# Kernel tuning notes

Hardware: AMD Instinct MI355X
Metric: run time of the kernel (lower is better)

Reference implementation:

```python
import jax, jax.numpy as jnp
import numpy as np

_NF4_LUT = jnp.array([-1.0, -0.6961928, -0.525073, -0.39491748, -0.28444138,
                      -0.18477343, -0.09105602, 0.0, 0.07958029, 0.1609302,
                      0.2461123, 0.33791524, 0.44070983, 0.56261897,
                      0.72295684, 1.0], dtype=jnp.float32)

IN_FEATURES = 4096


def dequantize_nf4(weight_q, scale, in_dim):
    # weight_q: (out, in_dim//2) bytes (stored as int32, values 0..255)
    high = (weight_q >> 4) & 15
    low = weight_q & 15
    n_out = weight_q.shape[0]
    # interleave: [h0, l0, h1, l1, ...] matching torch's 0::2 / 1::2 assignment
    idx = jnp.stack([high, low], axis=-1).reshape(n_out, -1)[:, :in_dim]
    return _NF4_LUT[idx] * scale[:, None]  # (out, in) float32


def setup_inputs() -> dict:
    key = jax.random.key(0)
    k1, k2, k3, k4 = jax.random.split(key, 4)
    x = jax.random.normal(k1, (2, 2048, 4096), dtype=jnp.float32)
    weight_q = jax.random.randint(k2, (11008, 2048), 0, 256, dtype=jnp.int32)
    scale = jax.random.uniform(k3, (11008,), dtype=jnp.float32)
    bias = jax.random.normal(k4, (11008,), dtype=jnp.float32)
    return {"x": x, "weight_q": weight_q, "scale": scale, "bias": bias}


def reference(x, weight_q, scale, bias):
    w = dequantize_nf4(weight_q, scale, IN_FEATURES)  # (out, in)
    # F.linear: x @ w.T + bias
    return jnp.einsum('bsi,oi->bso', x, w.astype(x.dtype)) + bias
```

## Files before the change

### kernel.cpp

```cpp
#include <hip/hip_runtime.h>
#include <stdint.h>

#define M_DIM 4096
#define K_DIM 4096
#define N_DIM 11008
#define KW_DIM 2048

typedef __bf16 bf16x8 __attribute__((ext_vector_type(8)));
typedef float  f32x4  __attribute__((ext_vector_type(4)));

typedef __attribute__((address_space(1))) const void gv_t;
typedef __attribute__((address_space(3))) void lv_t;

__device__ inline unsigned int bf16_rne_bits(float f) {
    unsigned int u = __float_as_uint(f);
    return (u + 0x7FFFu + ((u >> 16) & 1u)) >> 16;
}
__device__ inline unsigned int pack_bf16_pair(float lo, float hi) {
    return bf16_rne_bits(lo) | (bf16_rne_bits(hi) << 16);
}

#define NF4_INIT  {-1.0f, -0.6961928f, -0.525073f, -0.39491748f, \
                   -0.28444138f, -0.18477343f, -0.09105602f, 0.0f, \
                   0.07958029f, 0.1609302f, 0.2461123f, 0.33791524f, \
                   0.44070983f, 0.56261897f, 0.72295684f, 1.0f}

__global__ __launch_bounds__(256)
void dequant_w(const int4* __restrict__ Wq4, uint4* __restrict__ Wb4)
{
    __shared__ unsigned int lutr[256 * 32];
    const int t = threadIdx.x;
    {
        const float LUT[16] = NF4_INIT;
        const int c0 = t & 31;
        #pragma unroll
        for (int j = 0; j < 32; ++j) {
            const int e = (t >> 5) * 32 + j;
            lutr[e * 32 + c0] = pack_bf16_pair(LUT[(e >> 4) & 15], LUT[e & 15]);
        }
    }
    __syncthreads();
    const int c = t & 31;
    size_t gid = (size_t)blockIdx.x * 256 + t;
    const size_t stride = 2752u * 256u;
    #pragma unroll
    for (int it = 0; it < 8; ++it) {
        int4 w = Wq4[gid];
        uint4 o;
        o.x = lutr[(w.x & 255) * 32 + c];
        o.y = lutr[(w.y & 255) * 32 + c];
        o.z = lutr[(w.z & 255) * 32 + c];
        o.w = lutr[(w.w & 255) * 32 + c];
        Wb4[gid] = o;
        gid += stride;
    }
}

__global__ __launch_bounds__(256)
void convert_x(const float4* __restrict__ X4, uint4* __restrict__ Xb4)
{
    size_t gid = (size_t)blockIdx.x * 256 + threadIdx.x;
    float4 a = X4[gid * 2];
    float4 b = X4[gid * 2 + 1];
    uint4 o;
    o.x = pack_bf16_pair(a.x, a.y);
    o.y = pack_bf16_pair(a.z, a.w);
    o.z = pack_bf16_pair(b.x, b.y);
    o.w = pack_bf16_pair(b.z, b.w);
    Xb4[gid] = o;
}

constexpr int GBM = 256, GBN = 256, GBK = 32;
constexpr int NKT = K_DIM / GBK;
constexpr int NT2 = N_DIM / GBN;
constexpr int GRID2 = (M_DIM / GBM) * NT2;

__global__ __launch_bounds__(512, 2)
void gemm_8ph(const unsigned short* __restrict__ Xb, const unsigned short* __restrict__ Wb,
              const float* __restrict__ scale, const float* __restrict__ bias,
              float* __restrict__ Out)
{
    __shared__ __align__(16) char lds[131072];
    char* const ldsA = lds;
    char* const ldsB = lds + 65536;

    const int t = threadIdx.x;
    const int lane = t & 63;
    const int wv = t >> 6;
    const int wr = wv >> 2;
    const int wc = wv & 3;
    const int l16 = lane & 15, quad = lane >> 4;

    const int bid = blockIdx.x;
    const int wg = (bid & 7) * (GRID2 / 8) + (bid >> 3);
    const int m0 = (wg / NT2) * GBM;
    const int n0 = (wg % NT2) * GBN;

    const int sw  = ((quad ^ ((l16 >> 1) & 3)) << 4);
    const int a_rd = (wr * 128 + l16) * 64 + sw;
    const int b_rd = (wc * 64  + l16) * 64 + sw;

    const int srow  = t >> 2;
    const int sslot = (t & 3) ^ ((t >> 3) & 3);
    const unsigned short* sA = Xb + (size_t)(m0 + srow) * K_DIM + sslot * 8;
    const unsigned short* sB = Wb + (size_t)(n0 + srow) * K_DIM + sslot * 8;
    const int sdst = t * 16;

    f32x4 acc[8][4];
    #pragma unroll
    for (int i = 0; i < 8; ++i)
        #pragma unroll
        for (int j = 0; j < 4; ++j)
            acc[i][j] = f32x4{0.f, 0.f, 0.f, 0.f};

    #pragma unroll
    for (int k0 = 0; k0 < 3; ++k0) {
        char* Ad = ldsA + k0 * 16384;
        char* Bd = ldsB + k0 * 16384;
        __builtin_amdgcn_global_load_lds((gv_t*)(sA + k0 * 32),
                                         (lv_t*)(Ad + sdst), 16, 0, 0);
        __builtin_amdgcn_global_load_lds((gv_t*)(sA + k0 * 32 + (size_t)128 * K_DIM),
                                         (lv_t*)(Ad + 8192 + sdst), 16, 0, 0);
        __builtin_amdgcn_global_load_lds((gv_t*)(sB + k0 * 32),
                                         (lv_t*)(Bd + sdst), 16, 0, 0);
        __builtin_amdgcn_global_load_lds((gv_t*)(sB + k0 * 32 + (size_t)128 * K_DIM),
                                         (lv_t*)(Bd + 8192 + sdst), 16, 0, 0);
    }
    asm volatile("s_waitcnt vmcnt(8)" ::: "memory");
    __builtin_amdgcn_s_barrier();

    #pragma unroll 4
    for (int kt = 0; kt < NKT; ++kt) {
        const char* Ab = ldsA + (kt & 3) * 16384;
        const char* Bb = ldsB + (kt & 3) * 16384;
        const int ktS = (kt + 3 < NKT) ? (kt + 3) : (NKT - 1);
        char* AdS = ldsA + ((kt + 3) & 3) * 16384;
        char* BdS = ldsB + ((kt + 3) & 3) * 16384;

        bf16x8 af[4], bfr[4];

        #pragma unroll
        for (int i = 0; i < 4; ++i)
            af[i] = *reinterpret_cast<const bf16x8*>(Ab + a_rd + i * 1024);
        #pragma unroll
        for (int j = 0; j < 4; ++j)
            bfr[j] = *reinterpret_cast<const bf16x8*>(Bb + b_rd + j * 1024);
        __builtin_amdgcn_global_load_lds((gv_t*)(sA + ktS * 32),
                                         (lv_t*)(AdS + sdst), 16, 0, 0);
        __builtin_amdgcn_global_load_lds((gv_t*)(sA + ktS * 32 + (size_t)128 * K_DIM),
                                         (lv_t*)(AdS + 8192 + sdst), 16, 0, 0);
        __builtin_amdgcn_s_barrier();
        asm volatile("s_waitcnt lgkmcnt(0)" ::: "memory");
        __builtin_amdgcn_s_setprio(1);
        #pragma unroll
        for (int i = 0; i < 4; ++i)
            #pragma unroll
            for (int j = 0; j < 4; ++j)
                acc[i][j] = __builtin_amdgcn_mfma_f32_16x16x32_bf16(af[i], bfr[j], acc[i][j], 0, 0, 0);
        __builtin_amdgcn_s_setprio(0);
        __builtin_amdgcn_s_barrier();

        #pragma unroll
        for (int i = 0; i < 4; ++i)
            af[i] = *reinterpret_cast<const bf16x8*>(Ab + a_rd + 4096 + i * 1024);
        __builtin_amdgcn_global_load_lds((gv_t*)(sB + ktS * 32),
                                         (lv_t*)(BdS + sdst), 16, 0, 0);
        __builtin_amdgcn_global_load_lds((gv_t*)(sB + ktS * 32 + (size_t)128 * K_DIM),
                                         (lv_t*)(BdS + 8192 + sdst), 16, 0, 0);
        __builtin_amdgcn_s_barrier();
        asm volatile("s_waitcnt lgkmcnt(0)" ::: "memory");
        __builtin_amdgcn_s_setprio(1);
        #pragma unroll
        for (int i = 0; i < 4; ++i)
            #pragma unroll
            for (int j = 0; j < 4; ++j)
                acc[4 + i][j] = __builtin_amdgcn_mfma_f32_16x16x32_bf16(af[i], bfr[j], acc[4 + i][j], 0, 0, 0);
        __builtin_amdgcn_s_setprio(0);
        asm volatile("s_waitcnt vmcnt(8)" ::: "memory");
        __builtin_amdgcn_s_barrier();
    }

    asm volatile("s_waitcnt vmcnt(0)" ::: "memory");

    #pragma unroll
    for (int j = 0; j < 4; ++j) {
        const int n = n0 + wc * 64 + j * 16 + l16;
        const float s  = scale[n];
        const float bz = bias[n];
        #pragma unroll
        for (int ii = 0; ii < 8; ++ii) {
            const int m = m0 + wr * 128 + ii * 16 + quad * 4;
            float* op = Out + (size_t)m * N_DIM + n;
            #pragma unroll
            for (int r = 0; r < 4; ++r)
                op[(size_t)r * N_DIM] = acc[ii][j][r] * s + bz;
        }
    }
}

constexpr int BM = 128, BN = 128, BK = 64;
constexpr int F_LDK = BK + 8;
__global__ __launch_bounds__(256, 2)
void nf4_gemm_fused(const float* __restrict__ X, const int* __restrict__ Wq,
                    const float* __restrict__ scale, const float* __restrict__ bias,
                    float* __restrict__ Out)
{
    __shared__ __align__(16) unsigned short As[BM * F_LDK];
    __shared__ __align__(16) unsigned short Bs[BN * F_LDK];
    __shared__ unsigned int lut2[256];

    const int t = threadIdx.x;
    const int ntiles = N_DIM / BN;
    const int mtile = blockIdx.x / ntiles;
    const int ntile = blockIdx.x % ntiles;
    const int m0 = mtile * BM, n0 = ntile * BN;

    {
        const float LUT[16] = NF4_INIT;
        lut2[t] = pack_bf16_pair(LUT[(t >> 4) & 15], LUT[t & 15]);
    }

    const int lane = t & 63;
    const int wv = t >> 6;
    const int wr = wv >> 1, wc = wv & 1;
    const int l16 = lane & 15, quad = lane >> 4;

    const int a_r = t >> 4, a_c = (t & 15) * 4;
    const int b_r = t >> 3, b_c = (t & 7) * 4;

    const float* aptr = X + (m0 + a_r) * K_DIM + a_c;
    const int*   bptr = Wq + (n0 + b_r) * KW_DIM + b_c;

    f32x4 acc[4][4];
    #pragma unroll
    for (int i = 0; i < 4; ++i)
        #pragma unroll
        for (int j = 0; j < 4; ++j)
            acc[i][j] = f32x4{0.f, 0.f, 0.f, 0.f};

    for (int kt = 0; kt < K_DIM / BK; ++kt) {
        float4 av[8];
        int4   bv[4];
        #pragma unroll
        for (int i = 0; i < 8; ++i)
            av[i] = *reinterpret_cast<const float4*>(aptr + i * 16 * K_DIM);
        #pragma unroll
        for (int i = 0; i < 4; ++i)
            bv[i] = *reinterpret_cast<const int4*>(bptr + i * 32 * KW_DIM);
        aptr += BK;
        bptr += BK / 2;

        __syncthreads();

        #pragma unroll
        for (int i = 0; i < 8; ++i) {
            uint2 p;
            p.x = pack_bf16_pair(av[i].x, av[i].y);
            p.y = pack_bf16_pair(av[i].z, av[i].w);
            *reinterpret_cast<uint2*>(&As[(a_r + i * 16) * F_LDK + a_c]) = p;
        }
        #pragma unroll
        for (int i = 0; i < 4; ++i) {
            uint4 q;
            q.x = lut2[bv[i].x & 255];
            q.y = lut2[bv[i].y & 255];
            q.z = lut2[bv[i].z & 255];
            q.w = lut2[bv[i].w & 255];
            *reinterpret_cast<uint4*>(&Bs[(b_r + i * 32) * F_LDK + b_c * 2]) = q;
        }
        __syncthreads();

        #pragma unroll
        for (int ks = 0; ks < 2; ++ks) {
            bf16x8 af[4], bfr[4];
            const int kb = ks * 32 + quad * 8;
            #pragma unroll
            for (int i = 0; i < 4; ++i)
                af[i] = *reinterpret_cast<const bf16x8*>(&As[(wr * 64 + i * 16 + l16) * F_LDK + kb]);
            #pragma unroll
            for (int j = 0; j < 4; ++j)
                bfr[j] = *reinterpret_cast<const bf16x8*>(&Bs[(wc * 64 + j * 16 + l16) * F_LDK + kb]);
            #pragma unroll
            for (int i = 0; i < 4; ++i)
                #pragma unroll
                for (int j = 0; j < 4; ++j)
                    acc[i][j] = __builtin_amdgcn_mfma_f32_16x16x32_bf16(af[i], bfr[j], acc[i][j], 0, 0, 0);
        }
    }

    #pragma unroll
    for (int j = 0; j < 4; ++j) {
        const int n = n0 + wc * 64 + j * 16 + l16;
        const float s  = scale[n];
        const float bz = bias[n];
        #pragma unroll
        for (int i = 0; i < 4; ++i) {
            const int m = m0 + wr * 64 + i * 16 + quad * 4;
            float* op = Out + (size_t)m * N_DIM + n;
            #pragma unroll
            for (int r = 0; r < 4; ++r)
                op[(size_t)r * N_DIM] = acc[i][j][r] * s + bz;
        }
    }
}

extern "C" void kernel_launch(void* const* d_in, const int* in_sizes, int n_in,
                              void* d_out, int out_size, void* d_ws, size_t ws_size,
                              hipStream_t stream) {
    const float* X     = (const float*)d_in[0];
    const int*   Wq    = (const int*)d_in[1];
    const float* scale = (const float*)d_in[2];
    const float* bias  = (const float*)d_in[3];
    float* Out = (float*)d_out;

    const size_t WB_BYTES = (size_t)N_DIM * K_DIM * 2;
    const size_t XB_BYTES = (size_t)M_DIM * K_DIM * 2;

    if (ws_size >= WB_BYTES + XB_BYTES) {
        unsigned short* Wb = (unsigned short*)d_ws;
        unsigned short* Xb = (unsigned short*)((char*)d_ws + WB_BYTES);
        dequant_w<<<2752, 256, 0, stream>>>((const int4*)Wq, (uint4*)Wb);
        convert_x<<<8192, 256, 0, stream>>>((const float4*)X, (uint4*)Xb);
        gemm_8ph<<<GRID2, 512, 0, stream>>>(Xb, Wb, scale, bias, Out);
    } else {
        nf4_gemm_fused<<<(M_DIM / BM) * (N_DIM / BN), 256, 0, stream>>>(X, Wq, scale, bias, Out);
    }
}
```

Before: 611.1 us.

## Switch GEMM to BK=64 double-buffered LDS pipeline with 8-slot XOR swizzle

Replaces the 4-stage BK=32 LDS ring, which had split phases and several barriers per k-step, with a 2-stage BK=64 double buffer. Each k-step prefetches the next 64-wide tile of A and B into the other buffer, then runs two K-halves of MFMAs with a single barrier at the end. The LDS swizzle changes to an 8-slot XOR pattern to suit 128-byte rows. This halves the loop trip count and cuts barrier and waitcnt overhead, at the cost of shallower prefetch and less latency hiding.

```diff
diff --git a/kernel.cpp b/kernel.cpp
--- a/kernel.cpp
+++ b/kernel.cpp
@@ -70,15 +70,15 @@
     Xb4[gid] = o;
 }
 
-constexpr int GBM = 256, GBN = 256, GBK = 32;
+constexpr int GBM = 256, GBN = 256, GBK = 64;
 constexpr int NKT = K_DIM / GBK;
 constexpr int NT2 = N_DIM / GBN;
 constexpr int GRID2 = (M_DIM / GBM) * NT2;
 
 __global__ __launch_bounds__(512, 2)
-void gemm_8ph(const unsigned short* __restrict__ Xb, const unsigned short* __restrict__ Wb,
-              const float* __restrict__ scale, const float* __restrict__ bias,
-              float* __restrict__ Out)
+void gemm_bk64(const unsigned short* __restrict__ Xb, const unsigned short* __restrict__ Wb,
+               const float* __restrict__ scale, const float* __restrict__ bias,
+               float* __restrict__ Out)
 {
     __shared__ __align__(16) char lds[131072];
     char* const ldsA = lds;
@@ -96,12 +96,14 @@
     const int m0 = (wg / NT2) * GBM;
     const int n0 = (wg % NT2) * GBN;
 
-    const int sw  = ((quad ^ ((l16 >> 1) & 3)) << 4);
-    const int a_rd = (wr * 128 + l16) * 64 + sw;
-    const int b_rd = (wc * 64  + l16) * 64 + sw;
-
-    const int srow  = t >> 2;
-    const int sslot = (t & 3) ^ ((t >> 3) & 3);
+    const int r7 = l16 & 7;
+    const int swz0 = ((0 + quad) ^ r7) << 4;
+    const int swz1 = ((4 + quad) ^ r7) << 4;
+    const int a_rd = (wr * 128 + l16) * 128;
+    const int b_rd = (wc * 64  + l16) * 128;
+
+    const int srow  = t >> 3;
+    const int sslot = (t & 7) ^ ((t >> 3) & 7);
     const unsigned short* sA = Xb + (size_t)(m0 + srow) * K_DIM + sslot * 8;
     const unsigned short* sB = Wb + (size_t)(n0 + srow) * K_DIM + sslot * 8;
     const int sdst = t * 16;
@@ -114,69 +116,83 @@
             acc[i][j] = f32x4{0.f, 0.f, 0.f, 0.f};
 
     #pragma unroll
-    for (int k0 = 0; k0 < 3; ++k0) {
-        char* Ad = ldsA + k0 * 16384;
-        char* Bd = ldsB + k0 * 16384;
-        __builtin_amdgcn_global_load_lds((gv_t*)(sA + k0 * 32),
-                                         (lv_t*)(Ad + sdst), 16, 0, 0);
-        __builtin_amdgcn_global_load_lds((gv_t*)(sA + k0 * 32 + (size_t)128 * K_DIM),
-                                         (lv_t*)(Ad + 8192 + sdst), 16, 0, 0);
-        __builtin_amdgcn_global_load_lds((gv_t*)(sB + k0 * 32),
-                                         (lv_t*)(Bd + sdst), 16, 0, 0);
-        __builtin_amdgcn_global_load_lds((gv_t*)(sB + k0 * 32 + (size_t)128 * K_DIM),
-                                         (lv_t*)(Bd + 8192 + sdst), 16, 0, 0);
-    }
-    asm volatile("s_waitcnt vmcnt(8)" ::: "memory");
-    __builtin_amdgcn_s_barrier();
-
-    #pragma unroll 4
+    for (int c = 0; c < 4; ++c)
+        __builtin_amdgcn_global_load_lds((gv_t*)(sA + (size_t)c * 64 * K_DIM),
+                                         (lv_t*)(ldsA + c * 8192 + sdst), 16, 0, 0);
+    #pragma unroll
+    for (int c = 0; c < 4; ++c)
+        __builtin_amdgcn_global_load_lds((gv_t*)(sB + (size_t)c * 64 * K_DIM),
+                                         (lv_t*)(ldsB + c * 8192 + sdst), 16, 0, 0);
+
+    #pragma unroll 2
     for (int kt = 0; kt < NKT; ++kt) {
-        const char* Ab = ldsA + (kt & 3) * 16384;
-        const char* Bb = ldsB + (kt & 3) * 16384;
-        const int ktS = (kt + 3 < NKT) ? (kt + 3) : (NKT - 1);
-        char* AdS = ldsA + ((kt + 3) & 3) * 16384;
-        char* BdS = ldsB + ((kt + 3) & 3) * 16384;
-
-        bf16x8 af[4], bfr[4];
-
-        #pragma unroll
-        for (int i = 0; i < 4; ++i)
-            af[i] = *reinterpret_cast<const bf16x8*>(Ab + a_rd + i * 1024);
-        #pragma unroll
-        for (int j = 0; j < 4; ++j)
-            bfr[j] = *reinterpret_cast<const bf16x8*>(Bb + b_rd + j * 1024);
-        __builtin_amdgcn_global_load_lds((gv_t*)(sA + ktS * 32),
-                                         (lv_t*)(AdS + sdst), 16, 0, 0);
-        __builtin_amdgcn_global_load_lds((gv_t*)(sA + ktS * 32 + (size_t)128 * K_DIM),
-                                         (lv_t*)(AdS + 8192 + sdst), 16, 0, 0);
+        const int cur = kt & 1;
+        const int kts = (kt + 1 < NKT) ? (kt + 1) : (NKT - 1);
+        char* Ad = ldsA + (cur ^ 1) * 32768;
+        char* Bd = ldsB + (cur ^ 1) * 32768;
+        #pragma unroll
+        for (int c = 0; c < 4; ++c)
+            __builtin_amdgcn_global_load_lds((gv_t*)(sA + kts * 64 + (size_t)c * 64 * K_DIM),
+                                             (lv_t*)(Ad + c * 8192 + sdst), 16, 0, 0);
+        #pragma unroll
+        for (int c = 0; c < 4; ++c)
+            __builtin_amdgcn_global_load_lds((gv_t*)(sB + kts * 64 + (size_t)c * 64 * K_DIM),
+                                             (lv_t*)(Bd + c * 8192 + sdst), 16, 0, 0);
+
+        asm volatile("s_waitcnt vmcnt(8)" ::: "memory");
         __builtin_amdgcn_s_barrier();
-        asm volatile("s_waitcnt lgkmcnt(0)" ::: "memory");
-        __builtin_amdgcn_s_setprio(1);
-        #pragma unroll
-        for (int i = 0; i < 4; ++i)
+
+        const char* Ab = ldsA + cur * 32768;
+        const char* Bb = ldsB + cur * 32768;
+
+        {
+            bf16x8 af[8], bfr[4];
+            #pragma unroll
+            for (int i = 0; i < 4; ++i)
+                af[i] = *reinterpret_cast<const bf16x8*>(Ab + a_rd + i * 2048 + swz0);
             #pragma unroll
             for (int j = 0; j < 4; ++j)
-                acc[i][j] = __builtin_amdgcn_mfma_f32_16x16x32_bf16(af[i], bfr[j], acc[i][j], 0, 0, 0);
-        __builtin_amdgcn_s_setprio(0);
-        __builtin_amdgcn_s_barrier();
-
-        #pragma unroll
-        for (int i = 0; i < 4; ++i)
-            af[i] = *reinterpret_cast<const bf16x8*>(Ab + a_rd + 4096 + i * 1024);
-        __builtin_amdgcn_global_load_lds((gv_t*)(sB + ktS * 32),
-                                         (lv_t*)(BdS + sdst), 16, 0, 0);
-        __builtin_amdgcn_global_load_lds((gv_t*)(sB + ktS * 32 + (size_t)128 * K_DIM),
-                                         (lv_t*)(BdS + 8192 + sdst), 16, 0, 0);
-        __builtin_amdgcn_s_barrier();
-        asm volatile("s_waitcnt lgkmcnt(0)" ::: "memory");
-        __builtin_amdgcn_s_setprio(1);
-        #pragma unroll
-        for (int i = 0; i < 4; ++i)
+                bfr[j] = *reinterpret_cast<const bf16x8*>(Bb + b_rd + j * 2048 + swz0);
+            #pragma unroll
+            for (int i = 0; i < 4; ++i)
+                af[4 + i] = *reinterpret_cast<const bf16x8*>(Ab + a_rd + 8192 + i * 2048 + swz0);
+            __builtin_amdgcn_s_setprio(1);
+            #pragma unroll
+            for (int i = 0; i < 4; ++i)
+                #pragma unroll
+                for (int j = 0; j < 4; ++j)
+                    acc[i][j] = __builtin_amdgcn_mfma_f32_16x16x32_bf16(af[i], bfr[j], acc[i][j], 0, 0, 0);
+            #pragma unroll
+            for (int i = 0; i < 4; ++i)
+                #pragma unroll
+                for (int j = 0; j < 4; ++j)
+                    acc[4 + i][j] = __builtin_amdgcn_mfma_f32_16x16x32_bf16(af[4 + i], bfr[j], acc[4 + i][j], 0, 0, 0);
+            __builtin_amdgcn_s_setprio(0);
+        }
+        {
+            bf16x8 af[8], bfr[4];
+            #pragma unroll
+            for (int i = 0; i < 4; ++i)
+                af[i] = *reinterpret_cast<const bf16x8*>(Ab + a_rd + i * 2048 + swz1);
             #pragma unroll
             for (int j = 0; j < 4; ++j)
-                acc[4 + i][j] = __builtin_amdgcn_mfma_f32_16x16x32_bf16(af[i], bfr[j], acc[4 + i][j], 0, 0, 0);
-        __builtin_amdgcn_s_setprio(0);
-        asm volatile("s_waitcnt vmcnt(8)" ::: "memory");
+                bfr[j] = *reinterpret_cast<const bf16x8*>(Bb + b_rd + j * 2048 + swz1);
+            #pragma unroll
+            for (int i = 0; i < 4; ++i)
+                af[4 + i] = *reinterpret_cast<const bf16x8*>(Ab + a_rd + 8192 + i * 2048 + swz1);
+            __builtin_amdgcn_s_setprio(1);
+            #pragma unroll
+            for (int i = 0; i < 4; ++i)
+                #pragma unroll
+                for (int j = 0; j < 4; ++j)
+                    acc[i][j] = __builtin_amdgcn_mfma_f32_16x16x32_bf16(af[i], bfr[j], acc[i][j], 0, 0, 0);
+            #pragma unroll
+            for (int i = 0; i < 4; ++i)
+                #pragma unroll
+                for (int j = 0; j < 4; ++j)
+                    acc[4 + i][j] = __builtin_amdgcn_mfma_f32_16x16x32_bf16(af[4 + i], bfr[j], acc[4 + i][j], 0, 0, 0);
+            __builtin_amdgcn_s_setprio(0);
+        }
         __builtin_amdgcn_s_barrier();
     }
 
@@ -321,7 +337,7 @@
         unsigned short* Xb = (unsigned short*)((char*)d_ws + WB_BYTES);
         dequant_w<<<2752, 256, 0, stream>>>((const int4*)Wq, (uint4*)Wb);
         convert_x<<<8192, 256, 0, stream>>>((const float4*)X, (uint4*)Xb);
-        gemm_8ph<<<GRID2, 512, 0, stream>>>(Xb, Wb, scale, bias, Out);
+        gemm_bk64<<<GRID2, 512, 0, stream>>>(Xb, Wb, scale, bias, Out);
     } else {
         nf4_gemm_fused<<<(M_DIM / BM) * (N_DIM / BN), 256, 0, stream>>>(X, Wq, scale, bias, Out);
     }
```

Result: slower. 641.1 us (+4.9%).

## Double-buffer MFMA fragments in registers and cut GEMM main-loop barriers

Applied to the files above, without the earlier changes.

The bf16 GEMM main loop becomes a manually unrolled four-phase macro. The A and B fragments for the next k-tile are read from LDS into a second register buffer while the current tile's MFMAs run. Partial lgkmcnt waits with sched_barrier replace full lgkmcnt(0) waits, and the per-tile barrier count drops from three to one. The aim is to hide LDS read latency behind matrix math and remove synchronisation stalls, at the cost of more vector registers, which may spill or lower occupancy under the 512x2 launch bound.

```diff
diff --git a/kernel.cpp b/kernel.cpp
--- a/kernel.cpp
+++ b/kernel.cpp
@@ -76,9 +76,9 @@
 constexpr int GRID2 = (M_DIM / GBM) * NT2;
 
 __global__ __launch_bounds__(512, 2)
-void gemm_8ph(const unsigned short* __restrict__ Xb, const unsigned short* __restrict__ Wb,
-              const float* __restrict__ scale, const float* __restrict__ bias,
-              float* __restrict__ Out)
+void gemm_r4(const unsigned short* __restrict__ Xb, const unsigned short* __restrict__ Wb,
+             const float* __restrict__ scale, const float* __restrict__ bias,
+             float* __restrict__ Out)
 {
     __shared__ __align__(16) char lds[131072];
     char* const ldsA = lds;
@@ -96,9 +96,9 @@
     const int m0 = (wg / NT2) * GBM;
     const int n0 = (wg % NT2) * GBN;
 
-    const int sw  = ((quad ^ ((l16 >> 1) & 3)) << 4);
-    const int a_rd = (wr * 128 + l16) * 64 + sw;
-    const int b_rd = (wc * 64  + l16) * 64 + sw;
+    const int swz = ((quad ^ ((l16 >> 1) & 3)) << 4);
+    const int a_rd = (wr * 128 + l16) * 64 + swz;
+    const int b_rd = (wc * 64  + l16) * 64 + swz;
 
     const int srow  = t >> 2;
     const int sslot = (t & 3) ^ ((t >> 3) & 3);
@@ -113,72 +113,93 @@
         for (int j = 0; j < 4; ++j)
             acc[i][j] = f32x4{0.f, 0.f, 0.f, 0.f};
 
-    #pragma unroll
-    for (int k0 = 0; k0 < 3; ++k0) {
-        char* Ad = ldsA + k0 * 16384;
-        char* Bd = ldsB + k0 * 16384;
-        __builtin_amdgcn_global_load_lds((gv_t*)(sA + k0 * 32),
+    bf16x8 a0[2][4], bfrag[2][4], a1[4];
+
+    #pragma unroll
+    for (int c = 0; c < 3; ++c) {
+        char* Ad = ldsA + c * 16384;
+        char* Bd = ldsB + c * 16384;
+        __builtin_amdgcn_global_load_lds((gv_t*)(sA + c * 32),
                                          (lv_t*)(Ad + sdst), 16, 0, 0);
-        __builtin_amdgcn_global_load_lds((gv_t*)(sA + k0 * 32 + (size_t)128 * K_DIM),
+        __builtin_amdgcn_global_load_lds((gv_t*)(sA + c * 32 + (size_t)128 * K_DIM),
                                          (lv_t*)(Ad + 8192 + sdst), 16, 0, 0);
-        __builtin_amdgcn_global_load_lds((gv_t*)(sB + k0 * 32),
+        __builtin_amdgcn_global_load_lds((gv_t*)(sB + c * 32),
                                          (lv_t*)(Bd + sdst), 16, 0, 0);
-        __builtin_amdgcn_global_load_lds((gv_t*)(sB + k0 * 32 + (size_t)128 * K_DIM),
+        __builtin_amdgcn_global_load_lds((gv_t*)(sB + c * 32 + (size_t)128 * K_DIM),
                                          (lv_t*)(Bd + 8192 + sdst), 16, 0, 0);
     }
-    asm volatile("s_waitcnt vmcnt(8)" ::: "memory");
+    asm volatile("s_waitcnt vmcnt(4)" ::: "memory");
     __builtin_amdgcn_s_barrier();
 
-    #pragma unroll 4
-    for (int kt = 0; kt < NKT; ++kt) {
-        const char* Ab = ldsA + (kt & 3) * 16384;
-        const char* Bb = ldsB + (kt & 3) * 16384;
-        const int ktS = (kt + 3 < NKT) ? (kt + 3) : (NKT - 1);
-        char* AdS = ldsA + ((kt + 3) & 3) * 16384;
-        char* BdS = ldsB + ((kt + 3) & 3) * 16384;
-
-        bf16x8 af[4], bfr[4];
-
-        #pragma unroll
-        for (int i = 0; i < 4; ++i)
-            af[i] = *reinterpret_cast<const bf16x8*>(Ab + a_rd + i * 1024);
-        #pragma unroll
-        for (int j = 0; j < 4; ++j)
-            bfr[j] = *reinterpret_cast<const bf16x8*>(Bb + b_rd + j * 1024);
-        __builtin_amdgcn_global_load_lds((gv_t*)(sA + ktS * 32),
-                                         (lv_t*)(AdS + sdst), 16, 0, 0);
-        __builtin_amdgcn_global_load_lds((gv_t*)(sA + ktS * 32 + (size_t)128 * K_DIM),
-                                         (lv_t*)(AdS + 8192 + sdst), 16, 0, 0);
-        __builtin_amdgcn_s_barrier();
-        asm volatile("s_waitcnt lgkmcnt(0)" ::: "memory");
-        __builtin_amdgcn_s_setprio(1);
-        #pragma unroll
-        for (int i = 0; i < 4; ++i)
-            #pragma unroll
-            for (int j = 0; j < 4; ++j)
-                acc[i][j] = __builtin_amdgcn_mfma_f32_16x16x32_bf16(af[i], bfr[j], acc[i][j], 0, 0, 0);
-        __builtin_amdgcn_s_setprio(0);
-        __builtin_amdgcn_s_barrier();
-
-        #pragma unroll
-        for (int i = 0; i < 4; ++i)
-            af[i] = *reinterpret_cast<const bf16x8*>(Ab + a_rd + 4096 + i * 1024);
-        __builtin_amdgcn_global_load_lds((gv_t*)(sB + ktS * 32),
-                                         (lv_t*)(BdS + sdst), 16, 0, 0);
-        __builtin_amdgcn_global_load_lds((gv_t*)(sB + ktS * 32 + (size_t)128 * K_DIM),
-                                         (lv_t*)(BdS + 8192 + sdst), 16, 0, 0);
-        __builtin_amdgcn_s_barrier();
-        asm volatile("s_waitcnt lgkmcnt(0)" ::: "memory");
-        __builtin_amdgcn_s_setprio(1);
-        #pragma unroll
-        for (int i = 0; i < 4; ++i)
-            #pragma unroll
-            for (int j = 0; j < 4; ++j)
-                acc[4 + i][j] = __builtin_amdgcn_mfma_f32_16x16x32_bf16(af[i], bfr[j], acc[4 + i][j], 0, 0, 0);
-        __builtin_amdgcn_s_setprio(0);
-        asm volatile("s_waitcnt vmcnt(8)" ::: "memory");
-        __builtin_amdgcn_s_barrier();
-    }
+    #pragma unroll
+    for (int i = 0; i < 4; ++i)
+        a0[0][i] = *reinterpret_cast<const bf16x8*>(ldsA + a_rd + i * 1024);
+    #pragma unroll
+    for (int j = 0; j < 4; ++j)
+        bfrag[0][j] = *reinterpret_cast<const bf16x8*>(ldsB + b_rd + j * 1024);
+
+#define TILE(KT, PH)                                                                 \
+  {                                                                                  \
+    const char* Abuf = ldsA + (PH) * 16384;                                          \
+    char* AdS = ldsA + (((PH) + 3) & 3) * 16384;                                     \
+    char* BdS = ldsB + (((PH) + 3) & 3) * 16384;                                     \
+    const char* Anx = ldsA + (((PH) + 1) & 3) * 16384;                               \
+    const char* Bnx = ldsB + (((PH) + 1) & 3) * 16384;                               \
+    const int kts = ((KT) + 3 < NKT) ? ((KT) + 3) : (NKT - 1);                       \
+                    \
+    __builtin_amdgcn_global_load_lds((gv_t*)(sA + kts * 32),                         \
+                                     (lv_t*)(AdS + sdst), 16, 0, 0);                 \
+    __builtin_amdgcn_global_load_lds((gv_t*)(sA + kts * 32 + (size_t)128 * K_DIM),   \
+                                     (lv_t*)(AdS + 8192 + sdst), 16, 0, 0);          \
+    _Pragma("unroll")                                                                \
+    for (int i = 0; i < 4; ++i)                                                      \
+      a1[i] = *reinterpret_cast<const bf16x8*>(Abuf + a_rd + 4096 + i * 1024);       \
+    asm volatile("s_waitcnt lgkmcnt(4)" ::: "memory");                               \
+    __builtin_amdgcn_sched_barrier(0);                                               \
+    __builtin_amdgcn_s_setprio(1);                                                   \
+    _Pragma("unroll")                                                                \
+    for (int i = 0; i < 4; ++i)                                                      \
+      _Pragma("unroll")                                                              \
+      for (int j = 0; j < 4; ++j)                                                    \
+        acc[i][j] = __builtin_amdgcn_mfma_f32_16x16x32_bf16(a0[(PH) & 1][i],         \
+                        bfrag[(PH) & 1][j], acc[i][j], 0, 0, 0);                     \
+    __builtin_amdgcn_s_setprio(0);                                                   \
+                \
+    __builtin_amdgcn_global_load_lds((gv_t*)(sB + kts * 32),                         \
+                                     (lv_t*)(BdS + sdst), 16, 0, 0);                 \
+    __builtin_amdgcn_global_load_lds((gv_t*)(sB + kts * 32 + (size_t)128 * K_DIM),   \
+                                     (lv_t*)(BdS + 8192 + sdst), 16, 0, 0);          \
+    _Pragma("unroll")                                                                \
+    for (int i = 0; i < 4; ++i)                                                      \
+      a0[((PH) + 1) & 1][i] = *reinterpret_cast<const bf16x8*>(Anx + a_rd + i * 1024); \
+    _Pragma("unroll")                                                                \
+    for (int j = 0; j < 4; ++j)                                                      \
+      bfrag[((PH) + 1) & 1][j] = *reinterpret_cast<const bf16x8*>(Bnx + b_rd + j * 1024); \
+    asm volatile("s_waitcnt lgkmcnt(8)" ::: "memory");                               \
+    __builtin_amdgcn_sched_barrier(0);                                               \
+    __builtin_amdgcn_s_setprio(1);                                                   \
+    _Pragma("unroll")                                                                \
+    for (int i = 0; i < 4; ++i)                                                      \
+      _Pragma("unroll")                                                              \
+      for (int j = 0; j < 4; ++j)                                                    \
+        acc[4 + i][j] = __builtin_amdgcn_mfma_f32_16x16x32_bf16(a1[i],               \
+                        bfrag[(PH) & 1][j], acc[4 + i][j], 0, 0, 0);                 \
+    __builtin_amdgcn_s_setprio(0);                                                   \
+    asm volatile("s_waitcnt vmcnt(4)" ::: "memory");                                 \
+    __builtin_amdgcn_s_barrier();                                                    \
+  }
+
+    for (int kt4 = 0; kt4 < NKT; kt4 += 4) {
+        TILE(kt4 + 0, 0)
+        TILE(kt4 + 1, 1)
+        TILE(kt4 + 2, 2)
+        TILE(kt4 + 3, 3)
+    }
+#undef TILE
+
+    #pragma unroll
+    for (int i = 0; i < 4; ++i)
+        asm volatile("" :: "v"(a0[0][i]), "v"(bfrag[0][i]), "v"(a1[i]));
 
     asm volatile("s_waitcnt vmcnt(0)" ::: "memory");
 
@@ -321,7 +342,7 @@
         unsigned short* Xb = (unsigned short*)((char*)d_ws + WB_BYTES);
         dequant_w<<<2752, 256, 0, stream>>>((const int4*)Wq, (uint4*)Wb);
         convert_x<<<8192, 256, 0, stream>>>((const float4*)X, (uint4*)Xb);
-        gemm_8ph<<<GRID2, 512, 0, stream>>>(Xb, Wb, scale, bias, Out);
+        gemm_r4<<<GRID2, 512, 0, stream>>>(Xb, Wb, scale, bias, Out);
     } else {
         nf4_gemm_fused<<<(M_DIM / BM) * (N_DIM / BN), 256, 0, stream>>>(X, Wq, scale, bias, Out);
     }
```

Result: no change. 609.2 us (-0.3%).
